# Kernel optimization log

Measured on AMD Instinct MI355X. Metric: run time of the kernel, lower is better.

Reference implementation:

```python
import jax, jax.numpy as jnp
import numpy as np

N = 100000   # nodes
E = 800000   # edges
IN = 256     # input feature dim
H = 4        # heads per layer
D = 32       # per-head hidden dim (num_hidden)
SLOPE = 0.2  # leaky_relu negative slope


def setup_inputs() -> dict:
    key = jax.random.key(0)
    ks = jax.random.split(key, 8)
    s = 0.1  # weight scale for numerical stability
    x = jax.random.normal(ks[0], (N, IN), jnp.float32)
    edge_index = jax.random.randint(ks[1], (2, E), 0, N, dtype=jnp.int32)
    W0 = jax.random.normal(ks[2], (IN, H * D), jnp.float32) * s
    al0 = jax.random.normal(ks[3], (H, D), jnp.float32) * s
    ar0 = jax.random.normal(ks[4], (H, D), jnp.float32) * s
    W1 = jax.random.normal(ks[5], (H * D, H * D), jnp.float32) * s
    al1 = jax.random.normal(ks[6], (H, D), jnp.float32) * s
    ar1 = jax.random.normal(ks[7], (H, D), jnp.float32) * s
    return {"x": x, "edge_index": edge_index, "W0": W0, "al0": al0,
            "ar0": ar0, "W1": W1, "al1": al1, "ar1": ar1}


def _gat_layer(h, W, al, ar, src, dst, residual):
    """One GATConv: project, edge attention, dst-wise softmax, scatter-agg."""
    n = h.shape[0]
    feat = (h @ W).reshape(n, H, D)              # [N,H,D]
    el = jnp.einsum('nhd,hd->nh', feat, al)      # [N,H]
    er = jnp.einsum('nhd,hd->nh', feat, ar)      # [N,H]
    e = jax.nn.leaky_relu(el[src] + er[dst], SLOPE)   # raw scores [E,H]
    # edge softmax grouped by destination node (numerically stable)
    emax = jax.ops.segment_max(e, dst, num_segments=n)   # [N,H]
    eexp = jnp.exp(e - emax[dst])                          # [E,H]
    denom = jax.ops.segment_sum(eexp, dst, num_segments=n)  # [N,H]
    a = eexp / denom[dst]                                  # attention [E,H]
    msg = feat[src] * a[:, :, None]                        # [E,H,D]
    rst = jax.ops.segment_sum(msg, dst, num_segments=n)    # [N,H,D]
    if residual:
        rst = rst + h.reshape(n, H, D)  # identity residual (dims match)
    rst = jax.nn.elu(rst)               # activation
    return rst, a, e


def reference(x, edge_index, W0, al0, ar0, W1, al1, ar1):
    src, dst = edge_index[0], edge_index[1]
    # layer 0: no residual
    h1, a0, e0 = _gat_layer(x, W0, al0, ar0, src, dst, residual=False)
    atten0 = e0.mean(axis=-1)  # e_gat.flatten(1).mean(-1) -> [E]
    # layer 1: residual
    h2, a1, e1 = _gat_layer(h1.reshape(N, H * D), W1, al1, ar1, src, dst,
                            residual=True)
    atten1 = e1.mean(axis=-1)
    temp = h2.reshape(N, H * D)          # flattened node embeddings
    heads = tuple(h2[:, i] for i in range(H))  # per-head [N,D]
    return (temp,) + heads + (e1, atten0, atten1)
```

## Files before the change

### kernel.cpp

```cpp
#include <hip/hip_runtime.h>
#include <hip/hip_bf16.h>


typedef _Float16 f16;
typedef _Float16 f16x8 __attribute__((ext_vector_type(8)));
typedef float f32x4 __attribute__((ext_vector_type(4)));

__global__ void wsplit(const float* __restrict__ W, f16* __restrict__ Wth,
                       f16* __restrict__ Wtl, int K) {
    int i = blockIdx.x * blockDim.x + threadIdx.x;
    if (i >= K * 128) return;
    int k = i >> 7, c = i & 127;
    float v = W[i];
    f16 h = (f16)v;
    f16 l = (f16)(v - (float)h);
    Wth[(size_t)c * K + k] = h;
    Wtl[(size_t)c * K + k] = l;
}

__global__ __launch_bounds__(256, 2) void gemm_mfma(
        const float* __restrict__ X, const f16* __restrict__ Wth,
        const f16* __restrict__ Wtl, f16* __restrict__ Y16,
        const float* __restrict__ al, const float* __restrict__ ar,
        float* __restrict__ el_out, float* __restrict__ er_out,
        int nrows, int K) {
    constexpr int STR = 40;
    __shared__ f16 ash[128 * STR];
    __shared__ f16 asl[128 * STR];
    __shared__ f16 bsh[128 * STR];
    __shared__ f16 bsl[128 * STR];
    const int t    = threadIdx.x;
    const int wave = t >> 6;
    const int lane = t & 63;
    const int lr   = lane & 15;
    const int kg   = lane >> 4;
    const int row0 = blockIdx.x * 128;

    const int sr  = t >> 1;
    const int sko = (t & 1) * 16;
    const int ps  = ((sr & 7) << 4) | (sr >> 3);
    int gr = row0 + sr; if (gr >= nrows) gr = nrows - 1;

    f32x4 acc[2][8];
    #pragma unroll
    for (int i = 0; i < 2; ++i)
        #pragma unroll
        for (int j = 0; j < 8; ++j) acc[i][j] = (f32x4){0.f, 0.f, 0.f, 0.f};

    for (int k0 = 0; k0 < K; k0 += 32) {
        {
            const float* xp = X + (size_t)gr * K + k0 + sko;
            float4 v0 = *(const float4*)(xp + 0);
            float4 v1 = *(const float4*)(xp + 4);
            float4 v2 = *(const float4*)(xp + 8);
            float4 v3 = *(const float4*)(xp + 12);
            float vv[16] = {v0.x, v0.y, v0.z, v0.w, v1.x, v1.y, v1.z, v1.w,
                            v2.x, v2.y, v2.z, v2.w, v3.x, v3.y, v3.z, v3.w};
            f16x8 H0, H1, L0, L1;
            #pragma unroll
            for (int i = 0; i < 8; ++i) {
                f16 h0 = (f16)vv[i];
                H0[i] = h0;
                L0[i] = (f16)(vv[i] - (float)h0);
                f16 h1 = (f16)vv[i + 8];
                H1[i] = h1;
                L1[i] = (f16)(vv[i + 8] - (float)h1);
            }
            *(f16x8*)&ash[sr * STR + sko]     = H0;
            *(f16x8*)&ash[sr * STR + sko + 8] = H1;
            *(f16x8*)&asl[sr * STR + sko]     = L0;
            *(f16x8*)&asl[sr * STR + sko + 8] = L1;
        }
        {
            const f16* bph = Wth + (size_t)sr * K + k0 + sko;
            const f16* bpl = Wtl + (size_t)sr * K + k0 + sko;
            f16x8 b0 = *(const f16x8*)(bph);
            f16x8 b1 = *(const f16x8*)(bph + 8);
            f16x8 b2 = *(const f16x8*)(bpl);
            f16x8 b3 = *(const f16x8*)(bpl + 8);
            *(f16x8*)&bsh[ps * STR + sko]     = b0;
            *(f16x8*)&bsh[ps * STR + sko + 8] = b1;
            *(f16x8*)&bsl[ps * STR + sko]     = b2;
            *(f16x8*)&bsl[ps * STR + sko + 8] = b3;
        }
        __syncthreads();

        const int arow = wave * 32 + lr;
        f16x8 ah0 = *(const f16x8*)&ash[arow * STR + kg * 8];
        f16x8 ah1 = *(const f16x8*)&ash[(arow + 16) * STR + kg * 8];
        f16x8 al0 = *(const f16x8*)&asl[arow * STR + kg * 8];
        f16x8 al1 = *(const f16x8*)&asl[(arow + 16) * STR + kg * 8];
        f16x8 bh[8];
        #pragma unroll
        for (int cb = 0; cb < 8; ++cb)
            bh[cb] = *(const f16x8*)&bsh[(cb * 16 + lr) * STR + kg * 8];

        #pragma unroll
        for (int cb = 0; cb < 8; ++cb) {
            acc[0][cb] = __builtin_amdgcn_mfma_f32_16x16x32_f16(ah0, bh[cb], acc[0][cb], 0, 0, 0);
            acc[1][cb] = __builtin_amdgcn_mfma_f32_16x16x32_f16(ah1, bh[cb], acc[1][cb], 0, 0, 0);
        }
        #pragma unroll
        for (int cb = 0; cb < 8; ++cb) {
            acc[0][cb] = __builtin_amdgcn_mfma_f32_16x16x32_f16(al0, bh[cb], acc[0][cb], 0, 0, 0);
            acc[1][cb] = __builtin_amdgcn_mfma_f32_16x16x32_f16(al1, bh[cb], acc[1][cb], 0, 0, 0);
        }
        #pragma unroll
        for (int cb = 0; cb < 8; ++cb) {
            f16x8 bl = *(const f16x8*)&bsl[(cb * 16 + lr) * STR + kg * 8];
            acc[0][cb] = __builtin_amdgcn_mfma_f32_16x16x32_f16(ah0, bl, acc[0][cb], 0, 0, 0);
            acc[1][cb] = __builtin_amdgcn_mfma_f32_16x16x32_f16(ah1, bl, acc[1][cb], 0, 0, 0);
        }
        __syncthreads();
    }

    const int hh = lr >> 2;
    const int co = (lr & 3) * 8;
    float alv[8], arv[8];
    #pragma unroll
    for (int j = 0; j < 8; ++j) {
        alv[j] = al[hh * 32 + co + j];
        arv[j] = ar[hh * 32 + co + j];
    }
    #pragma unroll
    for (int rb = 0; rb < 2; ++rb) {
        int rbase = row0 + wave * 32 + rb * 16 + kg * 4;
        #pragma unroll
        for (int r = 0; r < 4; ++r) {
            int grow = rbase + r;
            f16x8 hv;
            float sl_ = 0.0f, sr_ = 0.0f;
            #pragma unroll
            for (int cb = 0; cb < 8; ++cb) {
                float v = acc[rb][cb][r];
                hv[cb] = (f16)v;
                sl_ += v * alv[cb];
                sr_ += v * arv[cb];
            }
            sl_ += __shfl_xor(sl_, 1); sl_ += __shfl_xor(sl_, 2);
            sr_ += __shfl_xor(sr_, 1); sr_ += __shfl_xor(sr_, 2);
            if (grow < nrows) {
                *(f16x8*)(Y16 + (size_t)grow * 128 + lr * 8) = hv;
                if ((lane & 3) == 0) {
                    el_out[4 * (size_t)grow + hh] = sl_;
                    er_out[4 * (size_t)grow + hh] = sr_;
                }
            }
        }
    }
}

__global__ void count_deg(const int* __restrict__ dsts, int* __restrict__ deg, int E) {
    int e = blockIdx.x * blockDim.x + threadIdx.x;
    if (e < E) atomicAdd(&deg[dsts[e]], 1);
}

__global__ __launch_bounds__(256) void scan_block(const int* __restrict__ deg,
                                                  int* __restrict__ excl,
                                                  int* __restrict__ bsums, int n) {
    __shared__ int wsums[4];
    int t = threadIdx.x;
    int base = blockIdx.x * 1024;
    int idx = base + t * 4;
    int v[4];
    #pragma unroll
    for (int i = 0; i < 4; ++i) v[i] = (idx + i < n) ? deg[idx + i] : 0;
    int tsum = v[0] + v[1] + v[2] + v[3];
    int lane = t & 63, wid = t >> 6;
    int incl = tsum;
    #pragma unroll
    for (int off = 1; off < 64; off <<= 1) {
        int u = __shfl_up(incl, off, 64);
        if (lane >= off) incl += u;
    }
    if (lane == 63) wsums[wid] = incl;
    __syncthreads();
    if (t == 0) {
        int s = 0;
        #pragma unroll
        for (int w = 0; w < 4; ++w) { int x = wsums[w]; wsums[w] = s; s += x; }
    }
    __syncthreads();
    int ex = incl - tsum + wsums[wid];
    int run = ex;
    #pragma unroll
    for (int i = 0; i < 4; ++i) { if (idx + i < n) excl[idx + i] = run; run += v[i]; }
    if (t == 255) bsums[blockIdx.x] = ex + tsum;
}

__global__ __launch_bounds__(256) void scan_sums(int* __restrict__ bs, int nb) {
    __shared__ int wsums[4];
    int t = threadIdx.x;
    int v = (t < nb) ? bs[t] : 0;
    int lane = t & 63, wid = t >> 6;
    int incl = v;
    #pragma unroll
    for (int off = 1; off < 64; off <<= 1) {
        int u = __shfl_up(incl, off, 64);
        if (lane >= off) incl += u;
    }
    if (lane == 63) wsums[wid] = incl;
    __syncthreads();
    if (t == 0) {
        int s = 0;
        #pragma unroll
        for (int w = 0; w < 4; ++w) { int x = wsums[w]; wsums[w] = s; s += x; }
    }
    __syncthreads();
    if (t < nb) bs[t] = incl - v + wsums[wid];
}

__global__ void scan_finalize(int* __restrict__ row_off, const int* __restrict__ bsums,
                              int* __restrict__ cursor, int n) {
    int i = blockIdx.x * blockDim.x + threadIdx.x;
    if (i < n) {
        int v = row_off[i] + bsums[i >> 10];
        row_off[i] = v;
        cursor[i]  = v;
    }
}

__global__ void fill_csr_edge0(const int* __restrict__ srcs, const int* __restrict__ dsts,
                               int* __restrict__ cursor, int* __restrict__ csr_src,
                               const float* __restrict__ el, const float* __restrict__ er,
                               float* __restrict__ atten0, int E) {
    int e = blockIdx.x * blockDim.x + threadIdx.x;
    if (e >= E) return;
    int s = srcs[e], d = dsts[e];
    int p = atomicAdd(&cursor[d], 1);
    csr_src[p] = s;
    float4 elv = *(const float4*)(el + 4 * (size_t)s);
    float4 erv = *(const float4*)(er + 4 * (size_t)d);
    float v0 = elv.x + erv.x, v1 = elv.y + erv.y;
    float v2 = elv.z + erv.z, v3 = elv.w + erv.w;
    v0 = v0 > 0.0f ? v0 : 0.2f * v0;
    v1 = v1 > 0.0f ? v1 : 0.2f * v1;
    v2 = v2 > 0.0f ? v2 : 0.2f * v2;
    v3 = v3 > 0.0f ? v3 : 0.2f * v3;
    atten0[e] = (v0 + v1 + v2 + v3) * 0.25f;
}

__global__ void edge1_kernel(const int* __restrict__ srcs, const int* __restrict__ dsts,
                             const float* __restrict__ el, const float* __restrict__ er,
                             float* __restrict__ e1_out, float* __restrict__ atten1,
                             int E) {
    int e = blockIdx.x * blockDim.x + threadIdx.x;
    if (e >= E) return;
    int s = srcs[e], d = dsts[e];
    float4 elv = *(const float4*)(el + 4 * (size_t)s);
    float4 erv = *(const float4*)(er + 4 * (size_t)d);
    float v0 = elv.x + erv.x, v1 = elv.y + erv.y;
    float v2 = elv.z + erv.z, v3 = elv.w + erv.w;
    v0 = v0 > 0.0f ? v0 : 0.2f * v0;
    v1 = v1 > 0.0f ? v1 : 0.2f * v1;
    v2 = v2 > 0.0f ? v2 : 0.2f * v2;
    v3 = v3 > 0.0f ? v3 : 0.2f * v3;
    *(float4*)(e1_out + 4 * (size_t)e) = make_float4(v0, v1, v2, v3);
    atten1[e] = (v0 + v1 + v2 + v3) * 0.25f;
}

template <int LAYER>
__global__ __launch_bounds__(256) void aggregate(const int* __restrict__ row_off,
                                                 const int* __restrict__ deg,
                                                 const int* __restrict__ csr_src,
                                                 const float* __restrict__ el,
                                                 const float* __restrict__ er,
                                                 const f16* __restrict__ feat16,
                                                 const float* __restrict__ resid,
                                                 float* __restrict__ out0,
                                                 float* __restrict__ heads,
                                                 int N) {
    int wave = (blockIdx.x * 256 + threadIdx.x) >> 6;
    if (wave >= N) return;
    int lane = threadIdx.x & 63;
    int q  = lane >> 4;
    int sc = lane & 15;
    int h  = sc >> 2;
    int start = row_off[wave];
    int dc    = deg[wave];
    float er_h = er[4 * (size_t)wave + h];

    float acc[8];
    #pragma unroll
    for (int j = 0; j < 8; ++j) acc[j] = 0.0f;
    float dh = 0.0f;

    for (int cs = 0; cs < dc; cs += 64) {
        int act = dc - cs; if (act > 64) act = 64;
        int sl = (lane < act) ? csr_src[start + cs + lane] : 0;
        int i = 0;
        for (; i + 8 <= act; i += 8) {
            int s0 = __shfl(sl, i + q);
            int s1 = __shfl(sl, i + 4 + q);
            float x0 = el[4 * (size_t)s0 + h] + er_h;
            float x1 = el[4 * (size_t)s1 + h] + er_h;
            x0 = x0 > 0.0f ? x0 : 0.2f * x0;
            x1 = x1 > 0.0f ? x1 : 0.2f * x1;
            float w0 = __expf(x0);
            float w1 = __expf(x1);
            f16x8 f0 = *(const f16x8*)(feat16 + 128 * (size_t)s0 + sc * 8);
            f16x8 f1 = *(const f16x8*)(feat16 + 128 * (size_t)s1 + sc * 8);
            #pragma unroll
            for (int j = 0; j < 8; ++j) acc[j] += w0 * (float)f0[j];
            #pragma unroll
            for (int j = 0; j < 8; ++j) acc[j] += w1 * (float)f1[j];
            dh += w0 + w1;
        }
        for (; i < act; i += 4) {
            int e = i + q;
            bool on = e < act;
            int s = __shfl(sl, on ? e : 0);
            float x = el[4 * (size_t)s + h] + er_h;
            x = x > 0.0f ? x : 0.2f * x;
            float w = on ? __expf(x) : 0.0f;
            f16x8 fv = *(const f16x8*)(feat16 + 128 * (size_t)s + sc * 8);
            #pragma unroll
            for (int j = 0; j < 8; ++j) acc[j] += w * (float)fv[j];
            dh += w;
        }
    }

    #pragma unroll
    for (int j = 0; j < 8; ++j) {
        acc[j] += __shfl_xor(acc[j], 16);
        acc[j] += __shfl_xor(acc[j], 32);
    }
    dh += __shfl_xor(dh, 16);
    dh += __shfl_xor(dh, 32);

    float inv = (dc > 0) ? 1.0f / dh : 0.0f;
    float ax = (q == 0) ? acc[0] : (q == 1) ? acc[2] : (q == 2) ? acc[4] : acc[6];
    float ay = (q == 0) ? acc[1] : (q == 1) ? acc[3] : (q == 2) ? acc[5] : acc[7];
    ax *= inv; ay *= inv;
    int c0 = sc * 8 + q * 2;
    size_t o = 128 * (size_t)wave + c0;
    if (LAYER == 1) {
        float2 rv = *(const float2*)(resid + o);
        ax += rv.x; ay += rv.y;
    }
    ax = ax > 0.0f ? ax : __expf(ax) - 1.0f;
    ay = ay > 0.0f ? ay : __expf(ay) - 1.0f;
    *(float2*)(out0 + o) = make_float2(ax, ay);
    if (LAYER == 1) {
        *(float2*)(heads + (size_t)h * N * 32 + (size_t)wave * 32 + (c0 & 31)) =
            make_float2(ax, ay);
    }
}

extern "C" void kernel_launch(void* const* d_in, const int* in_sizes, int n_in,
                              void* d_out, int out_size, void* d_ws, size_t ws_size,
                              hipStream_t stream) {
    const float* x   = (const float*)d_in[0];
    const int*   ei  = (const int*)d_in[1];
    const float* W0  = (const float*)d_in[2];
    const float* al0 = (const float*)d_in[3];
    const float* ar0 = (const float*)d_in[4];
    const float* W1  = (const float*)d_in[5];
    const float* al1 = (const float*)d_in[6];
    const float* ar1 = (const float*)d_in[7];

    const int N = in_sizes[0] / 256;
    const int E = in_sizes[1] / 2;
    const size_t NF = (size_t)N * 128;

    const int* srcs = ei;
    const int* dsts = ei + E;

    float* out = (float*)d_out;
    float* ws  = (float*)d_ws;
    f16*   feat16 = (f16*)ws;
    float* h1   = ws + NF;
    float* el   = ws + 2 * NF;
    float* er   = el + (size_t)N * 4;
    f16*   wth  = (f16*)(er + (size_t)N * 4);
    f16*   wtl0 = wth + (size_t)128 * 256;
    f16*   wtl1 = wth + (size_t)128 * 128;
    int*   ints    = (int*)(wth + (size_t)2 * 128 * 256);
    int*   deg     = ints;
    int*   row_off = deg + N;
    int*   cursor  = row_off + N;
    int*   csr_src = cursor + N;
    int*   bsums   = csr_src + E;

    float* heads      = out + NF;
    float* e1_out     = out + 2 * NF;
    float* atten0_out = e1_out + (size_t)E * 4;
    float* atten1_out = atten0_out + E;

    hipMemsetAsync(deg, 0, (size_t)N * sizeof(int), stream);
    count_deg<<<(E + 255) / 256, 256, 0, stream>>>(dsts, deg, E);
    int nb = (N + 1023) / 1024;
    scan_block<<<nb, 256, 0, stream>>>(deg, row_off, bsums, N);
    scan_sums<<<1, 256, 0, stream>>>(bsums, nb);
    scan_finalize<<<(N + 255) / 256, 256, 0, stream>>>(row_off, bsums, cursor, N);

    const int gemm_blocks = (N + 127) / 128;
    const int agg_blocks  = (N + 3) / 4;

    wsplit<<<(256 * 128 + 255) / 256, 256, 0, stream>>>(W0, wth, wtl0, 256);
    gemm_mfma<<<gemm_blocks, 256, 0, stream>>>(x, wth, wtl0, feat16, al0, ar0,
                                               el, er, N, 256);
    fill_csr_edge0<<<(E + 255) / 256, 256, 0, stream>>>(srcs, dsts, cursor, csr_src,
                                                        el, er, atten0_out, E);
    aggregate<0><<<agg_blocks, 256, 0, stream>>>(row_off, deg, csr_src, el, er,
                                                 feat16, nullptr, h1, nullptr, N);

    wsplit<<<(128 * 128 + 255) / 256, 256, 0, stream>>>(W1, wth, wtl1, 128);
    gemm_mfma<<<gemm_blocks, 256, 0, stream>>>(h1, wth, wtl1, feat16, al1, ar1,
                                               el, er, N, 128);
    edge1_kernel<<<(E + 255) / 256, 256, 0, stream>>>(srcs, dsts, el, er,
                                                      e1_out, atten1_out, E);
    aggregate<1><<<agg_blocks, 256, 0, stream>>>(row_off, deg, csr_src, el, er,
                                                 feat16, h1, out, heads, N);
}
```

Before: 452.9 us.

## Store layer-0 output in fp16 and drop A-low split in layer-1 GEMM

The layer-0 aggregate now writes h1 as fp16 instead of fp32. The layer-1 GEMM reads this fp16 input directly, skipping the hi/lo split of A, which removes one third of its MFMAs and half of its A-side memory traffic. The residual add in layer 1 also reads the fp16 copy. Both weight splits are merged into a single launch at the start. The cost is precision: h1, the residual and the layer-1 GEMM input all lose mantissa bits compared with the fp32 reference.

Result: faster. 443.5 us (-2.1%).

```diff
diff --git a/kernel.cpp b/kernel.cpp
--- a/kernel.cpp
+++ b/kernel.cpp
@@ -3,30 +3,40 @@
 
 
 typedef _Float16 f16;
+typedef _Float16 f16x2 __attribute__((ext_vector_type(2)));
 typedef _Float16 f16x8 __attribute__((ext_vector_type(8)));
 typedef float f32x4 __attribute__((ext_vector_type(4)));
 
-__global__ void wsplit(const float* __restrict__ W, f16* __restrict__ Wth,
-                       f16* __restrict__ Wtl, int K) {
+__global__ void wsplit2(const float* __restrict__ W0, const float* __restrict__ W1,
+                        f16* __restrict__ Wth0, f16* __restrict__ Wtl0,
+                        f16* __restrict__ Wth1, f16* __restrict__ Wtl1) {
     int i = blockIdx.x * blockDim.x + threadIdx.x;
-    if (i >= K * 128) return;
-    int k = i >> 7, c = i & 127;
-    float v = W[i];
-    f16 h = (f16)v;
-    f16 l = (f16)(v - (float)h);
-    Wth[(size_t)c * K + k] = h;
-    Wtl[(size_t)c * K + k] = l;
-}
-
+    if (i < 256 * 128) {
+        int k = i >> 7, c = i & 127;
+        float v = W0[i];
+        f16 h = (f16)v;
+        Wth0[(size_t)c * 256 + k] = h;
+        Wtl0[(size_t)c * 256 + k] = (f16)(v - (float)h);
+    } else if (i < 256 * 128 + 128 * 128) {
+        int j = i - 256 * 128;
+        int k = j >> 7, c = j & 127;
+        float v = W1[j];
+        f16 h = (f16)v;
+        Wth1[(size_t)c * 128 + k] = h;
+        Wtl1[(size_t)c * 128 + k] = (f16)(v - (float)h);
+    }
+}
+
+template <int AFP16>
 __global__ __launch_bounds__(256, 2) void gemm_mfma(
-        const float* __restrict__ X, const f16* __restrict__ Wth,
+        const void* __restrict__ Xv, const f16* __restrict__ Wth,
         const f16* __restrict__ Wtl, f16* __restrict__ Y16,
         const float* __restrict__ al, const float* __restrict__ ar,
         float* __restrict__ el_out, float* __restrict__ er_out,
         int nrows, int K) {
     constexpr int STR = 40;
     __shared__ f16 ash[128 * STR];
-    __shared__ f16 asl[128 * STR];
+    __shared__ f16 asl[AFP16 ? 2 : 128 * STR];
     __shared__ f16 bsh[128 * STR];
     __shared__ f16 bsl[128 * STR];
     const int t    = threadIdx.x;
@@ -48,8 +58,8 @@
         for (int j = 0; j < 8; ++j) acc[i][j] = (f32x4){0.f, 0.f, 0.f, 0.f};
 
     for (int k0 = 0; k0 < K; k0 += 32) {
-        {
-            const float* xp = X + (size_t)gr * K + k0 + sko;
+        if constexpr (!AFP16) {
+            const float* xp = (const float*)Xv + (size_t)gr * K + k0 + sko;
             float4 v0 = *(const float4*)(xp + 0);
             float4 v1 = *(const float4*)(xp + 4);
             float4 v2 = *(const float4*)(xp + 8);
@@ -70,6 +80,12 @@
             *(f16x8*)&ash[sr * STR + sko + 8] = H1;
             *(f16x8*)&asl[sr * STR + sko]     = L0;
             *(f16x8*)&asl[sr * STR + sko + 8] = L1;
+        } else {
+            const f16* xp = (const f16*)Xv + (size_t)gr * K + k0 + sko;
+            f16x8 a0 = *(const f16x8*)(xp);
+            f16x8 a1 = *(const f16x8*)(xp + 8);
+            *(f16x8*)&ash[sr * STR + sko]     = a0;
+            *(f16x8*)&ash[sr * STR + sko + 8] = a1;
         }
         {
             const f16* bph = Wth + (size_t)sr * K + k0 + sko;
@@ -88,8 +104,6 @@
         const int arow = wave * 32 + lr;
         f16x8 ah0 = *(const f16x8*)&ash[arow * STR + kg * 8];
         f16x8 ah1 = *(const f16x8*)&ash[(arow + 16) * STR + kg * 8];
-        f16x8 al0 = *(const f16x8*)&asl[arow * STR + kg * 8];
-        f16x8 al1 = *(const f16x8*)&asl[(arow + 16) * STR + kg * 8];
         f16x8 bh[8];
         #pragma unroll
         for (int cb = 0; cb < 8; ++cb)
@@ -100,10 +114,14 @@
             acc[0][cb] = __builtin_amdgcn_mfma_f32_16x16x32_f16(ah0, bh[cb], acc[0][cb], 0, 0, 0);
             acc[1][cb] = __builtin_amdgcn_mfma_f32_16x16x32_f16(ah1, bh[cb], acc[1][cb], 0, 0, 0);
         }
-        #pragma unroll
-        for (int cb = 0; cb < 8; ++cb) {
-            acc[0][cb] = __builtin_amdgcn_mfma_f32_16x16x32_f16(al0, bh[cb], acc[0][cb], 0, 0, 0);
-            acc[1][cb] = __builtin_amdgcn_mfma_f32_16x16x32_f16(al1, bh[cb], acc[1][cb], 0, 0, 0);
+        if constexpr (!AFP16) {
+            f16x8 al0_ = *(const f16x8*)&asl[arow * STR + kg * 8];
+            f16x8 al1_ = *(const f16x8*)&asl[(arow + 16) * STR + kg * 8];
+            #pragma unroll
+            for (int cb = 0; cb < 8; ++cb) {
+                acc[0][cb] = __builtin_amdgcn_mfma_f32_16x16x32_f16(al0_, bh[cb], acc[0][cb], 0, 0, 0);
+                acc[1][cb] = __builtin_amdgcn_mfma_f32_16x16x32_f16(al1_, bh[cb], acc[1][cb], 0, 0, 0);
+            }
         }
         #pragma unroll
         for (int cb = 0; cb < 8; ++cb) {
@@ -266,8 +284,9 @@
                                                  const float* __restrict__ el,
                                                  const float* __restrict__ er,
                                                  const f16* __restrict__ feat16,
-                                                 const float* __restrict__ resid,
-                                                 float* __restrict__ out0,
+                                                 const f16* __restrict__ resid16,
+                                                 f16* __restrict__ out16,
+                                                 float* __restrict__ out32,
                                                  float* __restrict__ heads,
                                                  int N) {
     int wave = (blockIdx.x * 256 + threadIdx.x) >> 6;
@@ -335,13 +354,16 @@
     int c0 = sc * 8 + q * 2;
     size_t o = 128 * (size_t)wave + c0;
     if (LAYER == 1) {
-        float2 rv = *(const float2*)(resid + o);
-        ax += rv.x; ay += rv.y;
+        f16x2 rv = *(const f16x2*)(resid16 + o);
+        ax += (float)rv[0]; ay += (float)rv[1];
     }
     ax = ax > 0.0f ? ax : __expf(ax) - 1.0f;
     ay = ay > 0.0f ? ay : __expf(ay) - 1.0f;
-    *(float2*)(out0 + o) = make_float2(ax, ay);
-    if (LAYER == 1) {
+    if (LAYER == 0) {
+        f16x2 hv; hv[0] = (f16)ax; hv[1] = (f16)ay;
+        *(f16x2*)(out16 + o) = hv;
+    } else {
+        *(float2*)(out32 + o) = make_float2(ax, ay);
         *(float2*)(heads + (size_t)h * N * 32 + (size_t)wave * 32 + (c0 & 31)) =
             make_float2(ax, ay);
     }
@@ -367,15 +389,16 @@
     const int* dsts = ei + E;
 
     float* out = (float*)d_out;
-    float* ws  = (float*)d_ws;
-    f16*   feat16 = (f16*)ws;
-    float* h1   = ws + NF;
-    float* el   = ws + 2 * NF;
+    f16*   f16ws  = (f16*)d_ws;
+    f16*   feat16 = f16ws;
+    f16*   h1_16  = feat16 + NF;
+    float* el   = (float*)(h1_16 + NF);
     float* er   = el + (size_t)N * 4;
-    f16*   wth  = (f16*)(er + (size_t)N * 4);
-    f16*   wtl0 = wth + (size_t)128 * 256;
-    f16*   wtl1 = wth + (size_t)128 * 128;
-    int*   ints    = (int*)(wth + (size_t)2 * 128 * 256);
+    f16*   wth0 = (f16*)(er + (size_t)N * 4);
+    f16*   wtl0 = wth0 + (size_t)128 * 256;
+    f16*   wth1 = wtl0 + (size_t)128 * 256;
+    f16*   wtl1 = wth1 + (size_t)128 * 128;
+    int*   ints    = (int*)(wtl1 + (size_t)128 * 128);
     int*   deg     = ints;
     int*   row_off = deg + N;
     int*   cursor  = row_off + N;
@@ -386,6 +409,9 @@
     float* e1_out     = out + 2 * NF;
     float* atten0_out = e1_out + (size_t)E * 4;
     float* atten1_out = atten0_out + E;
+
+    const int wtot = 256 * 128 + 128 * 128;
+    wsplit2<<<(wtot + 255) / 256, 256, 0, stream>>>(W0, W1, wth0, wtl0, wth1, wtl1);
 
     hipMemsetAsync(deg, 0, (size_t)N * sizeof(int), stream);
     count_deg<<<(E + 255) / 256, 256, 0, stream>>>(dsts, deg, E);
@@ -397,19 +423,19 @@
     const int gemm_blocks = (N + 127) / 128;
     const int agg_blocks  = (N + 3) / 4;
 
-    wsplit<<<(256 * 128 + 255) / 256, 256, 0, stream>>>(W0, wth, wtl0, 256);
-    gemm_mfma<<<gemm_blocks, 256, 0, stream>>>(x, wth, wtl0, feat16, al0, ar0,
-                                               el, er, N, 256);
+    gemm_mfma<0><<<gemm_blocks, 256, 0, stream>>>(x, wth0, wtl0, feat16, al0, ar0,
+                                                  el, er, N, 256);
     fill_csr_edge0<<<(E + 255) / 256, 256, 0, stream>>>(srcs, dsts, cursor, csr_src,
                                                         el, er, atten0_out, E);
     aggregate<0><<<agg_blocks, 256, 0, stream>>>(row_off, deg, csr_src, el, er,
-                                                 feat16, nullptr, h1, nullptr, N);
-
-    wsplit<<<(128 * 128 + 255) / 256, 256, 0, stream>>>(W1, wth, wtl1, 128);
-    gemm_mfma<<<gemm_blocks, 256, 0, stream>>>(h1, wth, wtl1, feat16, al1, ar1,
-                                               el, er, N, 128);
+                                                 feat16, nullptr, h1_16, nullptr,
+                                                 nullptr, N);
+
+    gemm_mfma<1><<<gemm_blocks, 256, 0, stream>>>(h1_16, wth1, wtl1, feat16, al1, ar1,
+                                                  el, er, N, 128);
     edge1_kernel<<<(E + 255) / 256, 256, 0, stream>>>(srcs, dsts, el, er,
                                                       e1_out, atten1_out, E);
     aggregate<1><<<agg_blocks, 256, 0, stream>>>(row_off, deg, csr_src, el, er,
-                                                 feat16, h1, out, heads, N);
-}
+                                                 feat16, h1_16, nullptr, out,
+                                                 heads, N);
+}
```
